# Kernel tuning notes

Measured on AMD Instinct MI355X. Metric: run time of the kernel, lower is better.

The kernel has to match this reference:

```python
import jax, jax.numpy as jnp
import numpy as np

D_MODEL = 1024
HEAD_SIZE = 64
B, T = 4, 4096


def setup_inputs() -> dict:
    key = jax.random.key(0)
    k1, k2, k3, k4, k5, k6 = jax.random.split(key, 6)
    q = jax.random.normal(k1, (B, T, D_MODEL), dtype=jnp.float32)
    k = jax.random.normal(k2, (B, T, D_MODEL), dtype=jnp.float32)
    v = jax.random.normal(k3, (B, T, D_MODEL), dtype=jnp.float32)
    # bias-free Linear weights stored as [d_model, head_size] so proj = x @ W
    s = 1.0 / np.sqrt(D_MODEL)
    Wq = jax.random.uniform(k4, (D_MODEL, HEAD_SIZE), jnp.float32, -s, s)
    Wk = jax.random.uniform(k5, (D_MODEL, HEAD_SIZE), jnp.float32, -s, s)
    Wv = jax.random.uniform(k6, (D_MODEL, HEAD_SIZE), jnp.float32, -s, s)
    # [T,T] bool mask, True = keep (lower-triangular, exercises masking path)
    attn_mask = jnp.tril(jnp.ones((T, T), dtype=jnp.bool_))
    return {"q": q, "k": k, "v": v, "Wq": Wq, "Wk": Wk, "Wv": Wv,
            "attn_mask": attn_mask}


def reference(q, k, v, Wq, Wk, Wv, attn_mask):
    # projections: [B,T,d_model] @ [d_model,head] -> [B,T,head]
    qh = q @ Wq
    kh = k @ Wk
    vh = v @ Wv
    # raw scores [B,T,T]; attention_operation is Identity
    att = jnp.einsum('bqh,bkh->bqk', qh, kh)
    # mask BEFORE scaling (matches original; -inf/scale == -inf)
    att = jnp.where(attn_mask[None, :, :], att, -jnp.inf)
    scale = jnp.asarray(HEAD_SIZE ** 0.5, att.dtype)
    probs = jax.nn.softmax(att / scale, axis=-1)
    # dropout rate is 0.0 -> no-op
    return jnp.einsum('bqk,bkh->bqh', probs, vh)
```

## Files before the change

### kernel.cpp

```cpp
#include <hip/hip_runtime.h>
#include <hip/hip_fp16.h>

typedef _Float16 f16;
typedef __fp16 h16x2 __attribute__((ext_vector_type(2)));
typedef _Float16 f16x8 __attribute__((ext_vector_type(8)));
typedef _Float16 f16x4v __attribute__((ext_vector_type(4)));
typedef float f32x4 __attribute__((ext_vector_type(4)));
typedef float f32x16 __attribute__((ext_vector_type(16)));
typedef unsigned int u32;
typedef u32 u32x4 __attribute__((ext_vector_type(4)));

constexpr int DM = 1024;
constexpr int HS = 64;
constexpr int NBATCH = 4;
constexpr int T = 4096;
constexpr float CEXP = 0.18033688011112042f;

#if __has_builtin(__builtin_amdgcn_exp2f)
#define EXP2(x) __builtin_amdgcn_exp2f(x)
#else
#define EXP2(x) exp2f(x)
#endif

static __device__ __forceinline__ u32 pack2_f16(float a, float b) {
  union { f16 h[2]; u32 u; } cv;
  cv.h[0] = (f16)a; cv.h[1] = (f16)b;
  return cv.u;
}

static __device__ __forceinline__ f16x8 cvt8(const f32x4& a0, const f32x4& a1) {
  union { h16x2 p[4]; f16x8 v; } cv;
  cv.p[0] = __builtin_amdgcn_cvt_pkrtz(a0[0], a0[1]);
  cv.p[1] = __builtin_amdgcn_cvt_pkrtz(a0[2], a0[3]);
  cv.p[2] = __builtin_amdgcn_cvt_pkrtz(a1[0], a1[1]);
  cv.p[3] = __builtin_amdgcn_cvt_pkrtz(a1[2], a1[3]);
  return cv.v;
}

static __device__ __forceinline__ void gload_lds16(const void* g, void* l) {
  __builtin_amdgcn_global_load_lds(
      (__attribute__((address_space(1))) void*)(g),
      (__attribute__((address_space(3))) void*)(l), 16, 0, 0);
}

__global__ void wtrans_kernel(const float* __restrict__ Wq, const float* __restrict__ Wk,
                              const float* __restrict__ Wv, f16* __restrict__ WTf) {
  const int which = blockIdx.y;
  const float* __restrict__ W = (which == 0) ? Wq : ((which == 1) ? Wk : Wv);
  const int o8 = blockIdx.x * 256 + threadIdx.x;
  const int t = o8 >> 8;
  const int cb = (o8 >> 6) & 3;
  const int g = (o8 >> 4) & 3;
  const int q15 = o8 & 15;
  const int col = cb * 16 + q15;
  f16x8 v;
#pragma unroll
  for (int e = 0; e < 8; ++e) v[e] = (f16)W[(t * 32 + 8 * g + e) * 64 + col];
  *(f16x8*)(WTf + which * 65536 + o8 * 8) = v;
}

__global__ __launch_bounds__(256, 1) void proj_kernel(
    const float* __restrict__ xq, const float* __restrict__ xk, const float* __restrict__ xv,
    const f16* __restrict__ WTf, f16* __restrict__ qh, f16* __restrict__ kh,
    f16* __restrict__ vhT) {
  __shared__ __align__(16) char Bs[131072];

  const int which = blockIdx.y;
  const float* __restrict__ x = (which == 0) ? xq : ((which == 1) ? xk : xv);
  const int tid = threadIdx.x;
  const int lane = tid & 63, w = tid >> 6;
  const int q15 = lane & 15, g = lane >> 4;

  const char* __restrict__ wsrc = (const char*)(WTf + (size_t)which * 65536);
#pragma unroll
  for (int j = 0; j < 32; ++j)
    gload_lds16(wsrc + j * 4096 + w * 1024 + lane * 16, &Bs[j * 4096 + w * 1024]);
  __builtin_amdgcn_sched_barrier(0);

  const size_t abase = (size_t)((const char*)x +
      ((size_t)blockIdx.x * 256 + w * 16 + q15) * 4096 + 32 * g);

#define AISSUE(slot, G2)                                                        \
  {                                                                             \
    const size_t ab = abase + (size_t)((G2) >> 4) * 262144           \
                    + (size_t)((G2) & 15) * 256;                                \
    asm volatile("global_load_dwordx4 %0, %1, off"            : "=v"(ld[slot][0]) : "v"(ab)); \
    asm volatile("global_load_dwordx4 %0, %1, off offset:16"  : "=v"(ld[slot][1]) : "v"(ab)); \
    asm volatile("global_load_dwordx4 %0, %1, off offset:128" : "=v"(ld[slot][2]) : "v"(ab)); \
    asm volatile("global_load_dwordx4 %0, %1, off offset:144" : "=v"(ld[slot][3]) : "v"(ab)); \
  }

  f32x4 ld[8][4];
  AISSUE(0, 0) AISSUE(1, 1) AISSUE(2, 2) AISSUE(3, 3)

  asm volatile("s_waitcnt vmcnt(16)" ::: "memory");
  __builtin_amdgcn_sched_barrier(0);
  __builtin_amdgcn_s_barrier();
  __builtin_amdgcn_sched_barrier(0);

  f32x4 acc[4][4];
#pragma unroll
  for (int t = 0; t < 4; ++t)
#pragma unroll
    for (int cb = 0; cb < 4; ++cb) acc[t][cb] = (f32x4){0.f, 0.f, 0.f, 0.f};

#pragma unroll
  for (int G = 0; G < 64; ++G) {
    const int t = G >> 4, s = G & 15, slot = G & 7;
    if (G < 61)      asm volatile("s_waitcnt vmcnt(12)" ::: "memory");
    else if (G == 61) asm volatile("s_waitcnt vmcnt(8)" ::: "memory");
    else if (G == 62) asm volatile("s_waitcnt vmcnt(4)" ::: "memory");
    else              asm volatile("s_waitcnt vmcnt(0)" ::: "memory");
    __builtin_amdgcn_sched_barrier(0);
    if (G + 4 < 64) AISSUE((G + 4) & 7, G + 4)

    const f16x8 af0 = cvt8(ld[slot][0], ld[slot][1]);
    const f16x8 af1 = cvt8(ld[slot][2], ld[slot][3]);
    const char* bb = &Bs[0] + s * 8192 + lane * 16;
#pragma unroll
    for (int cb = 0; cb < 4; ++cb) {
      const f16x8 b0 = *(const f16x8*)(bb + cb * 1024);
      acc[t][cb] = __builtin_amdgcn_mfma_f32_16x16x32_f16(af0, b0, acc[t][cb], 0, 0, 0);
    }
#pragma unroll
    for (int cb = 0; cb < 4; ++cb) {
      const f16x8 b1 = *(const f16x8*)(bb + 4096 + cb * 1024);
      acc[t][cb] = __builtin_amdgcn_mfma_f32_16x16x32_f16(af1, b1, acc[t][cb], 0, 0, 0);
    }
  }
#undef AISSUE

#pragma unroll
  for (int t = 0; t < 4; ++t) {
    const int row0 = blockIdx.x * 256 + t * 64 + w * 16;
    if (which < 2) {
      f16* __restrict__ outp = (which == 0) ? qh : kh;
#pragma unroll
      for (int cb = 0; cb < 4; ++cb)
#pragma unroll
        for (int j = 0; j < 4; ++j)
          outp[(size_t)(row0 + 4 * g + j) * HS + cb * 16 + q15] = (f16)acc[t][cb][j];
    } else {
      const int b = row0 >> 12;
      const int t0 = (row0 & (T - 1)) + 4 * g;
#pragma unroll
      for (int cb = 0; cb < 4; ++cb) {
        f16x4v pv;
#pragma unroll
        for (int j = 0; j < 4; ++j) pv[j] = (f16)acc[t][cb][j];
        *(f16x4v*)(vhT + (size_t)b * HS * T + (size_t)(cb * 16 + q15) * T + t0) = pv;
      }
    }
  }
}

__global__ __launch_bounds__(512, 4) void attn_kernel(
    const f16* __restrict__ qh, const f16* __restrict__ kh,
    const f16* __restrict__ vhT, float* __restrict__ out) {
  __shared__ float sO[4][64][33];
  __shared__ float sMm[8][32];
  __shared__ float sLs[8][32];

  const int tid = threadIdx.x;
  const int lane = tid & 63, w = tid >> 6;
  const int q31 = lane & 31, hi = lane >> 5;

  const int id = blockIdx.x;
  const int b = (id & 7) >> 1;
  const int qt = 127 - 2 * (id >> 3) - (id & 1);
  const int q0 = qt * 32;

  const f16* __restrict__ kbase = kh + (size_t)b * T * HS;
  const f16* __restrict__ vbase = vhT + (size_t)b * HS * T;
  const f16* __restrict__ qp = qh + (size_t)(b * T + q0 + q31) * HS + 8 * hi;

  f16x8 qb[4];
#pragma unroll
  for (int kt = 0; kt < 4; ++kt) qb[kt] = *(const f16x8*)(qp + 16 * kt);

  f32x16 o0, o1;
#pragma unroll
  for (int i = 0; i < 16; ++i) { o0[i] = 0.f; o1[i] = 0.f; }
  float m = -1e30f, lsum = 0.f;

  const int nblk = qt + 1;
  for (int blk = w; blk < nblk; blk += 8) {
    const int kv0 = blk * 32;
    const f16* kr = kbase + (size_t)(kv0 + q31) * HS + 8 * hi;
    f16x8 ka0 = *(const f16x8*)(kr);
    f16x8 ka1 = *(const f16x8*)(kr + 16);
    f16x8 ka2 = *(const f16x8*)(kr + 32);
    f16x8 ka3 = *(const f16x8*)(kr + 48);

    f32x16 s;
#pragma unroll
    for (int i = 0; i < 16; ++i) s[i] = 0.f;
    s = __builtin_amdgcn_mfma_f32_32x32x16_f16(ka0, qb[0], s, 0, 0, 0);
    s = __builtin_amdgcn_mfma_f32_32x32x16_f16(ka1, qb[1], s, 0, 0, 0);
    s = __builtin_amdgcn_mfma_f32_32x32x16_f16(ka2, qb[2], s, 0, 0, 0);
    s = __builtin_amdgcn_mfma_f32_32x32x16_f16(ka3, qb[3], s, 0, 0, 0);

    const f16* vr = vbase + (size_t)q31 * T + kv0 + 8 * hi;
    f16x8 v00 = *(const f16x8*)(vr);
    f16x8 v01 = *(const f16x8*)(vr + 16);
    f16x8 v10 = *(const f16x8*)(vr + (size_t)32 * T);
    f16x8 v11 = *(const f16x8*)(vr + (size_t)32 * T + 16);

    if (blk == qt) {
#pragma unroll
      for (int r = 0; r < 16; ++r) {
        const int kl = (r & 3) + 8 * (r >> 2) + 4 * hi;
        if (kl > q31) s[r] = -1e30f;
      }
    }

    float pm = s[0];
#pragma unroll
    for (int r = 1; r < 16; ++r) pm = fmaxf(pm, s[r]);
    pm = fmaxf(pm, __shfl_xor(pm, 32));
    if (!__all(pm <= m + 32.f)) {
      const float mn = fmaxf(m, pm);
      const float r = EXP2((m - mn) * CEXP);
      lsum *= r;
#pragma unroll
      for (int i = 0; i < 16; ++i) { o0[i] *= r; o1[i] *= r; }
      m = mn;
    }

    float p[16];
    float ps = 0.f;
#pragma unroll
    for (int r = 0; r < 16; ++r) { p[r] = EXP2((s[r] - m) * CEXP); ps += p[r]; }
    ps += __shfl_xor(ps, 32);
    lsum += ps;

    u32 c[8], xg[8];
#pragma unroll
    for (int i = 0; i < 8; ++i) c[i] = pack2_f16(p[2 * i], p[2 * i + 1]);
#pragma unroll
    for (int i = 0; i < 8; ++i) xg[i] = (u32)__shfl_xor((int)c[i], 32);
    union { u32x4 u; f16x8 f; } f1, f2;
    f1.u = (u32x4){ hi ? xg[2] : c[0], hi ? xg[3] : c[1], hi ? c[2] : xg[0], hi ? c[3] : xg[1] };
    f2.u = (u32x4){ hi ? xg[6] : c[4], hi ? xg[7] : c[5], hi ? c[6] : xg[4], hi ? c[7] : xg[5] };

    o0 = __builtin_amdgcn_mfma_f32_32x32x16_f16(v00, f1.f, o0, 0, 0, 0);
    o0 = __builtin_amdgcn_mfma_f32_32x32x16_f16(v01, f2.f, o0, 0, 0, 0);
    o1 = __builtin_amdgcn_mfma_f32_32x32x16_f16(v10, f1.f, o1, 0, 0, 0);
    o1 = __builtin_amdgcn_mfma_f32_32x32x16_f16(v11, f2.f, o1, 0, 0, 0);
  }

  if (lane < 32) sMm[w][q31] = m;
  __syncthreads();
  float M = sMm[0][q31];
#pragma unroll
  for (int w2 = 1; w2 < 8; ++w2) M = fmaxf(M, sMm[w2][q31]);
  const float sc = EXP2((m - M) * CEXP);
  if (lane < 32) sLs[w][q31] = lsum * sc;
#pragma unroll
  for (int i = 0; i < 16; ++i) { o0[i] *= sc; o1[i] *= sc; }

  if (w >= 4) {
#pragma unroll
    for (int r = 0; r < 16; ++r) {
      const int d = (r & 3) + 8 * (r >> 2) + 4 * hi;
      sO[w - 4][d][q31] = o0[r];
      sO[w - 4][d + 32][q31] = o1[r];
    }
  }
  __syncthreads();
  if (w < 4) {
#pragma unroll
    for (int r = 0; r < 16; ++r) {
      const int d = (r & 3) + 8 * (r >> 2) + 4 * hi;
      sO[w][d][q31] += o0[r];
      sO[w][d + 32][q31] += o1[r];
    }
  }
  __syncthreads();

  const int q = tid >> 4;
  const int d0 = (tid & 15) * 4;
  float L = 0.f;
#pragma unroll
  for (int w2 = 0; w2 < 8; ++w2) L += sLs[w2][q];
  const float invL = 1.f / L;
  float4 rv;
  rv.x = (sO[0][d0 + 0][q] + sO[1][d0 + 0][q] + sO[2][d0 + 0][q] + sO[3][d0 + 0][q]) * invL;
  rv.y = (sO[0][d0 + 1][q] + sO[1][d0 + 1][q] + sO[2][d0 + 1][q] + sO[3][d0 + 1][q]) * invL;
  rv.z = (sO[0][d0 + 2][q] + sO[1][d0 + 2][q] + sO[2][d0 + 2][q] + sO[3][d0 + 2][q]) * invL;
  rv.w = (sO[0][d0 + 3][q] + sO[1][d0 + 3][q] + sO[2][d0 + 3][q] + sO[3][d0 + 3][q]) * invL;
  *(float4*)(out + (size_t)(b * T + q0 + q) * HS + d0) = rv;
}

extern "C" void kernel_launch(void* const* d_in, const int* in_sizes, int n_in,
                              void* d_out, int out_size, void* d_ws, size_t ws_size,
                              hipStream_t stream) {
  const float* q  = (const float*)d_in[0];
  const float* k  = (const float*)d_in[1];
  const float* v  = (const float*)d_in[2];
  const float* Wq = (const float*)d_in[3];
  const float* Wk = (const float*)d_in[4];
  const float* Wv = (const float*)d_in[5];
  float* out = (float*)d_out;

  f16* qh  = (f16*)d_ws;
  f16* kh  = qh  + (size_t)NBATCH * T * HS;
  f16* vhT = kh  + (size_t)NBATCH * T * HS;
  f16* WTf = vhT + (size_t)NBATCH * T * HS;

  wtrans_kernel<<<dim3(32, 3), 256, 0, stream>>>(Wq, Wk, Wv, WTf);
  proj_kernel<<<dim3(64, 3), 256, 0, stream>>>(q, k, v, WTf, qh, kh, vhT);
  attn_kernel<<<dim3(T / 32 * NBATCH), 512, 0, stream>>>(qh, kh, vhT, out);
}
```

Baseline: 89.30 us.

## Split projection into 256 row blocks each doing q, k, v phases sequentially

The projection grid changes from 64x3 blocks (each doing 256 rows of one input) to 256 blocks that each handle 64 rows and run three phases in turn for q, k and v. The weight tile is reloaded into LDS at every phase. The A-operand prefetch depth goes from 4 to 6 slots. This is meant to fill all compute units (256 CUs) instead of 192 blocks and to shorten the per-block tail. In exchange it loads the weights three times per block and adds barriers between phases.

```diff
diff --git a/kernel.cpp b/kernel.cpp
--- a/kernel.cpp
+++ b/kernel.cpp
@@ -65,93 +65,93 @@
     f16* __restrict__ vhT) {
   __shared__ __align__(16) char Bs[131072];
 
-  const int which = blockIdx.y;
-  const float* __restrict__ x = (which == 0) ? xq : ((which == 1) ? xk : xv);
   const int tid = threadIdx.x;
   const int lane = tid & 63, w = tid >> 6;
   const int q15 = lane & 15, g = lane >> 4;
-
-  const char* __restrict__ wsrc = (const char*)(WTf + (size_t)which * 65536);
-#pragma unroll
-  for (int j = 0; j < 32; ++j)
-    gload_lds16(wsrc + j * 4096 + w * 1024 + lane * 16, &Bs[j * 4096 + w * 1024]);
-  __builtin_amdgcn_sched_barrier(0);
-
-  const size_t abase = (size_t)((const char*)x +
-      ((size_t)blockIdx.x * 256 + w * 16 + q15) * 4096 + 32 * g);
+  const int row0 = blockIdx.x * 64;
 
 #define AISSUE(slot, G2)                                                        \
   {                                                                             \
-    const size_t ab = abase + (size_t)((G2) >> 4) * 262144           \
-                    + (size_t)((G2) & 15) * 256;                                \
+    const size_t ab = abase + (size_t)((G2) * 256);                             \
     asm volatile("global_load_dwordx4 %0, %1, off"            : "=v"(ld[slot][0]) : "v"(ab)); \
     asm volatile("global_load_dwordx4 %0, %1, off offset:16"  : "=v"(ld[slot][1]) : "v"(ab)); \
     asm volatile("global_load_dwordx4 %0, %1, off offset:128" : "=v"(ld[slot][2]) : "v"(ab)); \
     asm volatile("global_load_dwordx4 %0, %1, off offset:144" : "=v"(ld[slot][3]) : "v"(ab)); \
   }
 
-  f32x4 ld[8][4];
-  AISSUE(0, 0) AISSUE(1, 1) AISSUE(2, 2) AISSUE(3, 3)
-
-  asm volatile("s_waitcnt vmcnt(16)" ::: "memory");
-  __builtin_amdgcn_sched_barrier(0);
-  __builtin_amdgcn_s_barrier();
-  __builtin_amdgcn_sched_barrier(0);
-
-  f32x4 acc[4][4];
-#pragma unroll
-  for (int t = 0; t < 4; ++t)
-#pragma unroll
-    for (int cb = 0; cb < 4; ++cb) acc[t][cb] = (f32x4){0.f, 0.f, 0.f, 0.f};
-
-#pragma unroll
-  for (int G = 0; G < 64; ++G) {
-    const int t = G >> 4, s = G & 15, slot = G & 7;
-    if (G < 61)      asm volatile("s_waitcnt vmcnt(12)" ::: "memory");
-    else if (G == 61) asm volatile("s_waitcnt vmcnt(8)" ::: "memory");
-    else if (G == 62) asm volatile("s_waitcnt vmcnt(4)" ::: "memory");
-    else              asm volatile("s_waitcnt vmcnt(0)" ::: "memory");
-    __builtin_amdgcn_sched_barrier(0);
-    if (G + 4 < 64) AISSUE((G + 4) & 7, G + 4)
-
-    const f16x8 af0 = cvt8(ld[slot][0], ld[slot][1]);
-    const f16x8 af1 = cvt8(ld[slot][2], ld[slot][3]);
-    const char* bb = &Bs[0] + s * 8192 + lane * 16;
-#pragma unroll
-    for (int cb = 0; cb < 4; ++cb) {
-      const f16x8 b0 = *(const f16x8*)(bb + cb * 1024);
-      acc[t][cb] = __builtin_amdgcn_mfma_f32_16x16x32_f16(af0, b0, acc[t][cb], 0, 0, 0);
-    }
-#pragma unroll
-    for (int cb = 0; cb < 4; ++cb) {
-      const f16x8 b1 = *(const f16x8*)(bb + 4096 + cb * 1024);
-      acc[t][cb] = __builtin_amdgcn_mfma_f32_16x16x32_f16(af1, b1, acc[t][cb], 0, 0, 0);
-    }
-  }
+#define PHASE(WHICH, XP, FIRST)                                                 \
+  {                                                                             \
+    if (!(FIRST)) {                                                             \
+      asm volatile("s_waitcnt vmcnt(0)" ::: "memory");                          \
+      __builtin_amdgcn_sched_barrier(0);                                        \
+      __builtin_amdgcn_s_barrier();   \
+      __builtin_amdgcn_sched_barrier(0);                                        \
+    }                                                                           \
+                          \
+    {                                                                           \
+      const char* wsrc = (const char*)(WTf + (size_t)(WHICH) * 65536);          \
+      _Pragma("unroll") for (int j = 0; j < 32; ++j)                            \
+        gload_lds16(wsrc + j * 4096 + w * 1024 + lane * 16,                     \
+                    &Bs[j * 4096 + w * 1024]);                                  \
+      __builtin_amdgcn_sched_barrier(0);                                        \
+    }                                                                           \
+    const size_t abase = (size_t)((const char*)(XP) +                           \
+        (size_t)(row0 + w * 16 + q15) * 4096 + 32 * g);                         \
+    f32x4 ld[8][4];                                                             \
+    AISSUE(0, 0) AISSUE(1, 1) AISSUE(2, 2) AISSUE(3, 3) AISSUE(4, 4) AISSUE(5, 5) \
+    asm volatile("s_waitcnt vmcnt(24)" ::: "memory");             \
+    __builtin_amdgcn_sched_barrier(0);                                          \
+    __builtin_amdgcn_s_barrier();                                               \
+    __builtin_amdgcn_sched_barrier(0);                                          \
+    f32x4 acc[4];                                                               \
+    _Pragma("unroll") for (int cb = 0; cb < 4; ++cb)                            \
+      acc[cb] = (f32x4){0.f, 0.f, 0.f, 0.f};                                    \
+    _Pragma("unroll") for (int G = 0; G < 16; ++G) {                            \
+      if (G < 11)       asm volatile("s_waitcnt vmcnt(20)" ::: "memory");       \
+      else if (G == 11) asm volatile("s_waitcnt vmcnt(16)" ::: "memory");       \
+      else if (G == 12) asm volatile("s_waitcnt vmcnt(12)" ::: "memory");       \
+      else if (G == 13) asm volatile("s_waitcnt vmcnt(8)" ::: "memory");        \
+      else if (G == 14) asm volatile("s_waitcnt vmcnt(4)" ::: "memory");        \
+      else              asm volatile("s_waitcnt vmcnt(0)" ::: "memory");        \
+      __builtin_amdgcn_sched_barrier(0);                                        \
+      if (G + 6 < 16) AISSUE((G + 6) & 7, G + 6)                                \
+      const int slot = G & 7;                                                   \
+      const f16x8 af0 = cvt8(ld[slot][0], ld[slot][1]);                         \
+      const f16x8 af1 = cvt8(ld[slot][2], ld[slot][3]);                         \
+      const char* bb = &Bs[0] + G * 8192 + lane * 16;                           \
+      _Pragma("unroll") for (int cb = 0; cb < 4; ++cb) {                        \
+        const f16x8 b0 = *(const f16x8*)(bb + cb * 1024);                       \
+        acc[cb] = __builtin_amdgcn_mfma_f32_16x16x32_f16(af0, b0, acc[cb], 0, 0, 0); \
+      }                                                                         \
+      _Pragma("unroll") for (int cb = 0; cb < 4; ++cb) {                        \
+        const f16x8 b1 = *(const f16x8*)(bb + 4096 + cb * 1024);                \
+        acc[cb] = __builtin_amdgcn_mfma_f32_16x16x32_f16(af1, b1, acc[cb], 0, 0, 0); \
+      }                                                                         \
+    }                                                                           \
+                \
+    if ((WHICH) < 2) {                                                          \
+      f16* __restrict__ outp = ((WHICH) == 0) ? qh : kh;                        \
+      const int r0 = row0 + w * 16;                                             \
+      _Pragma("unroll") for (int cb = 0; cb < 4; ++cb)                          \
+        _Pragma("unroll") for (int j = 0; j < 4; ++j)                           \
+          outp[(size_t)(r0 + 4 * g + j) * HS + cb * 16 + q15] = (f16)acc[cb][j]; \
+    } else {                                                                    \
+      const int r0 = row0 + w * 16;                                             \
+      const int b = r0 >> 12;                                                   \
+      const int t0 = (r0 & (T - 1)) + 4 * g;                                    \
+      _Pragma("unroll") for (int cb = 0; cb < 4; ++cb) {                        \
+        f16x4v pv;                                                              \
+        _Pragma("unroll") for (int j = 0; j < 4; ++j) pv[j] = (f16)acc[cb][j];  \
+        *(f16x4v*)(vhT + (size_t)b * HS * T + (size_t)(cb * 16 + q15) * T + t0) = pv; \
+      }                                                                         \
+    }                                                                           \
+  }
+
+  PHASE(0, xq, true)
+  PHASE(1, xk, false)
+  PHASE(2, xv, false)
+#undef PHASE
 #undef AISSUE
-
-#pragma unroll
-  for (int t = 0; t < 4; ++t) {
-    const int row0 = blockIdx.x * 256 + t * 64 + w * 16;
-    if (which < 2) {
-      f16* __restrict__ outp = (which == 0) ? qh : kh;
-#pragma unroll
-      for (int cb = 0; cb < 4; ++cb)
-#pragma unroll
-        for (int j = 0; j < 4; ++j)
-          outp[(size_t)(row0 + 4 * g + j) * HS + cb * 16 + q15] = (f16)acc[t][cb][j];
-    } else {
-      const int b = row0 >> 12;
-      const int t0 = (row0 & (T - 1)) + 4 * g;
-#pragma unroll
-      for (int cb = 0; cb < 4; ++cb) {
-        f16x4v pv;
-#pragma unroll
-        for (int j = 0; j < 4; ++j) pv[j] = (f16)acc[t][cb][j];
-        *(f16x4v*)(vhT + (size_t)b * HS * T + (size_t)(cb * 16 + q15) * T + t0) = pv;
-      }
-    }
-  }
 }
 
 __global__ __launch_bounds__(512, 4) void attn_kernel(
@@ -309,6 +309,6 @@
   f16* WTf = vhT + (size_t)NBATCH * T * HS;
 
   wtrans_kernel<<<dim3(32, 3), 256, 0, stream>>>(Wq, Wk, Wv, WTf);
-  proj_kernel<<<dim3(64, 3), 256, 0, stream>>>(q, k, v, WTf, qh, kh, vhT);
+  proj_kernel<<<dim3(256), 256, 0, stream>>>(q, k, v, WTf, qh, kh, vhT);
   attn_kernel<<<dim3(T / 32 * NBATCH), 512, 0, stream>>>(qh, kh, vhT, out);
 }
```

Measured after the change: 91.31 us. +2.2%, slower.

## Stage converted fp16 A tiles through swizzled LDS and split output columns across waves

Applied to the files above, without the earlier changes.

The projection kernel now loads fp32 activations with coalesced row-contiguous reads. It converts them to fp16 and writes them into a double-buffered, XOR-swizzled LDS tile. Each wave then computes a 16-column slice of the output for all 256 rows, instead of its own 16 rows against all 64 columns. This is meant to improve global load coalescing and cut per-wave B fragment traffic, at the cost of an LDS round trip and a workgroup barrier on every k-step.

```diff
diff --git a/kernel.cpp b/kernel.cpp
--- a/kernel.cpp
+++ b/kernel.cpp
@@ -8,6 +8,7 @@
 typedef float f32x4 __attribute__((ext_vector_type(4)));
 typedef float f32x16 __attribute__((ext_vector_type(16)));
 typedef unsigned int u32;
+typedef u32 u32x2 __attribute__((ext_vector_type(2)));
 typedef u32 u32x4 __attribute__((ext_vector_type(4)));
 
 constexpr int DM = 1024;
@@ -28,13 +29,10 @@
   return cv.u;
 }
 
-static __device__ __forceinline__ f16x8 cvt8(const f32x4& a0, const f32x4& a1) {
-  union { h16x2 p[4]; f16x8 v; } cv;
-  cv.p[0] = __builtin_amdgcn_cvt_pkrtz(a0[0], a0[1]);
-  cv.p[1] = __builtin_amdgcn_cvt_pkrtz(a0[2], a0[3]);
-  cv.p[2] = __builtin_amdgcn_cvt_pkrtz(a1[0], a1[1]);
-  cv.p[3] = __builtin_amdgcn_cvt_pkrtz(a1[2], a1[3]);
-  return cv.v;
+static __device__ __forceinline__ u32 pkrtz(float a, float b) {
+  union { h16x2 h; u32 u; } cv;
+  cv.h = __builtin_amdgcn_cvt_pkrtz(a, b);
+  return cv.u;
 }
 
 static __device__ __forceinline__ void gload_lds16(const void* g, void* l) {
@@ -64,92 +62,121 @@
     const f16* __restrict__ WTf, f16* __restrict__ qh, f16* __restrict__ kh,
     f16* __restrict__ vhT) {
   __shared__ __align__(16) char Bs[131072];
+  __shared__ __align__(16) char Aw[2][8192];
 
   const int which = blockIdx.y;
   const float* __restrict__ x = (which == 0) ? xq : ((which == 1) ? xk : xv);
   const int tid = threadIdx.x;
   const int lane = tid & 63, w = tid >> 6;
   const int q15 = lane & 15, g = lane >> 4;
+  const int rowblk = blockIdx.x * 256;
 
   const char* __restrict__ wsrc = (const char*)(WTf + (size_t)which * 65536);
 #pragma unroll
-  for (int j = 0; j < 32; ++j)
-    gload_lds16(wsrc + j * 4096 + w * 1024 + lane * 16, &Bs[j * 4096 + w * 1024]);
+  for (int j = 0; j < 32; ++j) {
+    const int idx = j * 4 + w;
+    gload_lds16(wsrc + idx * 1024 + lane * 16, &Bs[idx * 1024]);
+  }
   __builtin_amdgcn_sched_barrier(0);
 
   const size_t abase = (size_t)((const char*)x +
-      ((size_t)blockIdx.x * 256 + w * 16 + q15) * 4096 + 32 * g);
-
-#define AISSUE(slot, G2)                                                        \
-  {                                                                             \
-    const size_t ab = abase + (size_t)((G2) >> 4) * 262144           \
-                    + (size_t)((G2) & 15) * 256;                                \
-    asm volatile("global_load_dwordx4 %0, %1, off"            : "=v"(ld[slot][0]) : "v"(ab)); \
-    asm volatile("global_load_dwordx4 %0, %1, off offset:16"  : "=v"(ld[slot][1]) : "v"(ab)); \
-    asm volatile("global_load_dwordx4 %0, %1, off offset:128" : "=v"(ld[slot][2]) : "v"(ab)); \
-    asm volatile("global_load_dwordx4 %0, %1, off offset:144" : "=v"(ld[slot][3]) : "v"(ab)); \
-  }
-
-  f32x4 ld[8][4];
+      ((size_t)rowblk + w * 4) * 4096 + lane * 16);
+  f32x4 ld[4][4];
+
+#define AISSUE(slot, S)                                                          \
+  {                                                                              \
+    const size_t ab = abase + (size_t)((S) >> 2) * 65536 + (size_t)((S) & 3) * 1024; \
+    asm volatile("global_load_dwordx4 %0, %1, off" : "=v"(ld[slot][0]) : "v"(ab));          \
+    asm volatile("global_load_dwordx4 %0, %1, off" : "=v"(ld[slot][1]) : "v"(ab + 4096));   \
+    asm volatile("global_load_dwordx4 %0, %1, off" : "=v"(ld[slot][2]) : "v"(ab + 8192));   \
+    asm volatile("global_load_dwordx4 %0, %1, off" : "=v"(ld[slot][3]) : "v"(ab + 12288));  \
+  }
+
+  int wb[4];
+#pragma unroll
+  for (int i = 0; i < 4; ++i) {
+    const int rw = w * 4 + i;
+    wb[i] = rw * 512 + (((lane >> 1) ^ (rw & 7)) * 16) + (lane & 1) * 8;
+  }
+
+#define AWRITE(slot, S)                                                          \
+  {                                                                              \
+    char* dst = &Aw[(S) & 1][0];                                                 \
+    _Pragma("unroll") for (int i = 0; i < 4; ++i) {                              \
+      u32x2 pv;                                                                  \
+      pv[0] = pkrtz(ld[slot][i][0], ld[slot][i][1]);                             \
+      pv[1] = pkrtz(ld[slot][i][2], ld[slot][i][3]);                             \
+      *(u32x2*)(dst + wb[i]) = pv;                                               \
+    }                                                                            \
+  }
+
+  f32x4 acc[16];
+#pragma unroll
+  for (int r = 0; r < 16; ++r) acc[r] = (f32x4){0.f, 0.f, 0.f, 0.f};
+
+  const int rx = q15 & 7;
+
+#define ACOMP(q)                                                                 \
+  {                                                                              \
+    const char* ab2 = &Aw[(q) & 1][0] + q15 * 512;                               \
+    _Pragma("unroll") for (int t = 0; t < 8; ++t) {                              \
+      const f16x8 af = *(const f16x8*)(ab2 + (((4 * t + g) ^ rx) * 16));         \
+      const f16x8 bf = *(const f16x8*)(&Bs[((((q) & 3) * 8 + t) * 4 + w) * 1024 + lane * 16]); \
+      acc[(q) >> 2] = __builtin_amdgcn_mfma_f32_16x16x32_f16(af, bf, acc[(q) >> 2], 0, 0, 0); \
+    }                                                                            \
+  }
+
   AISSUE(0, 0) AISSUE(1, 1) AISSUE(2, 2) AISSUE(3, 3)
-
-  asm volatile("s_waitcnt vmcnt(16)" ::: "memory");
+  asm volatile("s_waitcnt vmcnt(12)" ::: "memory");
+  __builtin_amdgcn_sched_barrier(0);
+  AWRITE(0, 0)
+  AISSUE(0, 4)
+  asm volatile("s_waitcnt lgkmcnt(0)" ::: "memory");
   __builtin_amdgcn_sched_barrier(0);
   __builtin_amdgcn_s_barrier();
   __builtin_amdgcn_sched_barrier(0);
 
-  f32x4 acc[4][4];
-#pragma unroll
-  for (int t = 0; t < 4; ++t)
-#pragma unroll
-    for (int cb = 0; cb < 4; ++cb) acc[t][cb] = (f32x4){0.f, 0.f, 0.f, 0.f};
-
-#pragma unroll
-  for (int G = 0; G < 64; ++G) {
-    const int t = G >> 4, s = G & 15, slot = G & 7;
-    if (G < 61)      asm volatile("s_waitcnt vmcnt(12)" ::: "memory");
-    else if (G == 61) asm volatile("s_waitcnt vmcnt(8)" ::: "memory");
-    else if (G == 62) asm volatile("s_waitcnt vmcnt(4)" ::: "memory");
-    else              asm volatile("s_waitcnt vmcnt(0)" ::: "memory");
+#pragma unroll
+  for (int q = 0; q < 64; ++q) {
+    if (q <= 59)      asm volatile("s_waitcnt vmcnt(12)" ::: "memory");
+    else if (q == 60) asm volatile("s_waitcnt vmcnt(8)" ::: "memory");
+    else if (q == 61) asm volatile("s_waitcnt vmcnt(4)" ::: "memory");
+    else if (q == 62) asm volatile("s_waitcnt vmcnt(0)" ::: "memory");
     __builtin_amdgcn_sched_barrier(0);
-    if (G + 4 < 64) AISSUE((G + 4) & 7, G + 4)
-
-    const f16x8 af0 = cvt8(ld[slot][0], ld[slot][1]);
-    const f16x8 af1 = cvt8(ld[slot][2], ld[slot][3]);
-    const char* bb = &Bs[0] + s * 8192 + lane * 16;
-#pragma unroll
-    for (int cb = 0; cb < 4; ++cb) {
-      const f16x8 b0 = *(const f16x8*)(bb + cb * 1024);
-      acc[t][cb] = __builtin_amdgcn_mfma_f32_16x16x32_f16(af0, b0, acc[t][cb], 0, 0, 0);
-    }
-#pragma unroll
-    for (int cb = 0; cb < 4; ++cb) {
-      const f16x8 b1 = *(const f16x8*)(bb + 4096 + cb * 1024);
-      acc[t][cb] = __builtin_amdgcn_mfma_f32_16x16x32_f16(af1, b1, acc[t][cb], 0, 0, 0);
-    }
+    if (q <= 62) {
+      const int slot = (q + 1) & 3;
+      AWRITE(slot, q + 1)
+      if (q + 5 <= 63) AISSUE(slot, q + 5)
+    }
+    ACOMP(q)
+    asm volatile("s_waitcnt lgkmcnt(0)" ::: "memory");
+    __builtin_amdgcn_sched_barrier(0);
+    __builtin_amdgcn_s_barrier();
+    __builtin_amdgcn_sched_barrier(0);
   }
 #undef AISSUE
-
-#pragma unroll
-  for (int t = 0; t < 4; ++t) {
-    const int row0 = blockIdx.x * 256 + t * 64 + w * 16;
-    if (which < 2) {
-      f16* __restrict__ outp = (which == 0) ? qh : kh;
-#pragma unroll
-      for (int cb = 0; cb < 4; ++cb)
-#pragma unroll
-        for (int j = 0; j < 4; ++j)
-          outp[(size_t)(row0 + 4 * g + j) * HS + cb * 16 + q15] = (f16)acc[t][cb][j];
-    } else {
-      const int b = row0 >> 12;
-      const int t0 = (row0 & (T - 1)) + 4 * g;
-#pragma unroll
-      for (int cb = 0; cb < 4; ++cb) {
-        f16x4v pv;
-#pragma unroll
-        for (int j = 0; j < 4; ++j) pv[j] = (f16)acc[t][cb][j];
-        *(f16x4v*)(vhT + (size_t)b * HS * T + (size_t)(cb * 16 + q15) * T + t0) = pv;
-      }
+#undef AWRITE
+#undef ACOMP
+
+  if (which < 2) {
+    f16* __restrict__ outp = (which == 0) ? qh : kh;
+#pragma unroll
+    for (int rg = 0; rg < 16; ++rg) {
+      const int row0 = rowblk + rg * 16;
+#pragma unroll
+      for (int j = 0; j < 4; ++j)
+        outp[(size_t)(row0 + 4 * g + j) * HS + w * 16 + q15] = (f16)acc[rg][j];
+    }
+  } else {
+    const int b = rowblk >> 12;
+    const int col = w * 16 + q15;
+#pragma unroll
+    for (int rg = 0; rg < 16; ++rg) {
+      const int t0 = ((rowblk + rg * 16) & (T - 1)) + 4 * g;
+      f16x4v pv;
+#pragma unroll
+      for (int j = 0; j < 4; ++j) pv[j] = (f16)acc[rg][j];
+      *(f16x4v*)(vhT + (size_t)b * HS * T + (size_t)col * T + t0) = pv;
     }
   }
 }
```

After: 89.35 us. No clear change (+0.0%).
